# Kernel tuning notes

Hardware: AMD Instinct MI355X
Metric: run time of the kernel (lower is better)

The kernel has to match this reference:

```python
import jax, jax.numpy as jnp
import numpy as np

DOWNSAMPLE_RATIO = 4  # init kwarg


def farthest_point_sample(pos, m):
    """PointNet++-style FPS. pos: [B,N,3] float. Returns int32 indices [B,m].
    Starts from point 0, iteratively picks the point with max min-distance to
    the already-selected set (squared euclidean), matching the CUDA kernel."""
    B, N, _ = pos.shape

    def step(carry, _):
        dist, last = carry                                   # [B,N], [B]
        p = jnp.take_along_axis(pos, last[:, None, None], axis=1)  # [B,1,3]
        d = jnp.sum((pos - p) ** 2, axis=-1)                 # [B,N]
        dist = jnp.minimum(dist, d)
        nxt = jnp.argmax(dist, axis=-1).astype(jnp.int32)    # [B]
        return (dist, nxt), nxt

    idx0 = jnp.zeros((B,), jnp.int32)
    dist0 = jnp.full((B, N), 1e10, dtype=pos.dtype)
    _, rest = jax.lax.scan(step, (dist0, idx0), None, length=m - 1)  # rest: [m-1,B]
    return jnp.concatenate([idx0[None, :], rest], axis=0).T  # [B,m]


def setup_inputs() -> dict:
    key = jax.random.key(0)
    k1, k2 = jax.random.split(key)
    B, N, C = 8, 16384, 256
    pos = jax.random.normal(k1, (B, N, 3), dtype=jnp.float32)
    feat = jax.random.normal(k2, (B, N, C), dtype=jnp.float32)
    return {"pos": pos, "feat": feat}


def reference(pos, feat):
    # fps_preprocess is None -> run FPS then gather (gather_operation == index
    # select along the point dim; the einsum transposes in the original cancel).
    B, N, _ = pos.shape
    m = N // DOWNSAMPLE_RATIO
    idx = farthest_point_sample(pos, m)                      # [B,m] int32
    pos_ds = jnp.take_along_axis(pos, idx[:, :, None], axis=1)   # [B,m,3]
    feat_ds = jnp.take_along_axis(feat, idx[:, :, None], axis=1)  # [B,m,C]
    return (pos_ds, feat_ds)
```

## Files before the change

kernel.cpp:

```cpp
#include <hip/hip_runtime.h>
#include <hip/hip_bf16.h>


constexpr int NPTS   = 16384;
constexpr int PTS    = 16;
constexpr int FPS_T  = 1024;
constexpr int WAVES  = FPS_T / 64;

template <int CTRL>
__device__ __forceinline__ float dpp_f(float x) {
    return __builtin_bit_cast(float,
        __builtin_amdgcn_update_dpp(0, __builtin_bit_cast(int, x), CTRL, 0xF, 0xF, true));
}
template <int CTRL>
__device__ __forceinline__ int dpp_i(int x) {
    return __builtin_amdgcn_update_dpp(0, x, CTRL, 0xF, 0xF, true);
}

__device__ __forceinline__ void permswap16_f(float &a, float &b) {
    asm volatile("v_permlane16_swap_b32 %0, %1" : "+v"(a), "+v"(b));
}
__device__ __forceinline__ void permswap16_i(int &a, int &b) {
    asm volatile("v_permlane16_swap_b32 %0, %1" : "+v"(a), "+v"(b));
}
__device__ __forceinline__ void permswap32_f(float &a, float &b) {
    asm volatile("v_permlane32_swap_b32 %0, %1" : "+v"(a), "+v"(b));
}
__device__ __forceinline__ void permswap32_i(int &a, int &b) {
    asm volatile("v_permlane32_swap_b32 %0, %1" : "+v"(a), "+v"(b));
}

__device__ __forceinline__ void take(float &v, int &i, float ov, int oi) {
    bool t = (ov > v) || (ov == v && oi < i);
    v = t ? ov : v;
    i = t ? oi : i;
}

__global__ __launch_bounds__(FPS_T)
__attribute__((amdgpu_waves_per_eu(4, 4)))
void fps_kernel(
    const float* __restrict__ pos,
    float* __restrict__ pos_out,
    int* __restrict__ idx_out,
    int m)
{
    const int b    = blockIdx.x;
    const int t    = threadIdx.x;
    const int lane = t & 63;
    const int wid  = t >> 6;
    const bool l16 = (lane & 16) != 0;
    const bool l32 = (lane & 32) != 0;
    const float* posb = pos + (size_t)b * NPTS * 3;

    __shared__ float  s_v[2][WAVES];
    __shared__ int    s_i[2][WAVES];
    __shared__ float2 sxy[NPTS];

    float pz[PTS], dist[PTS];
#pragma unroll
    for (int j = 0; j < PTS; ++j) {
        const int i = j * FPS_T + t;
        sxy[i]  = make_float2(posb[i * 3 + 0], posb[i * 3 + 1]);
        pz[j]   = posb[i * 3 + 2];
        dist[j] = 1e10f;
    }

    float lx = posb[0], ly = posb[1], lz = posb[2];

    if (t == 0) {
        idx_out[(size_t)b * m] = 0;
        pos_out[((size_t)b * m) * 3 + 0] = lx;
        pos_out[((size_t)b * m) * 3 + 1] = ly;
        pos_out[((size_t)b * m) * 3 + 2] = lz;
    }
    __syncthreads();

    for (int s = 1; s < m; ++s) {
        float bv = -1.0f;
        int   bj = 0;
        {
#pragma clang fp contract(off)
#pragma unroll
            for (int j = 0; j < PTS; ++j) {
                float2 xy = sxy[j * FPS_T + t];
                float dx = xy.x - lx;
                float dy = xy.y - ly;
                float dz = pz[j] - lz;
                float d  = ((dx * dx) + (dy * dy)) + (dz * dz);
                float nd = fminf(dist[j], d);
                dist[j]  = nd;
                if (nd > bv) { bv = nd; bj = j; }
            }
        }
        int bi = bj * FPS_T + t;

        take(bv, bi, dpp_f<0xB1>(bv),  dpp_i<0xB1>(bi));
        take(bv, bi, dpp_f<0x4E>(bv),  dpp_i<0x4E>(bi));
        take(bv, bi, dpp_f<0x141>(bv), dpp_i<0x141>(bi));
        take(bv, bi, dpp_f<0x140>(bv), dpp_i<0x140>(bi));
        {
            float a = bv, c = bv; permswap16_f(a, c);
            int   e = bi, f = bi; permswap16_i(e, f);
            take(bv, bi, l16 ? a : c, l16 ? e : f);
        }
        {
            float a = bv, c = bv; permswap32_f(a, c);
            int   e = bi, f = bi; permswap32_i(e, f);
            take(bv, bi, l32 ? a : c, l32 ? e : f);
        }

        const int buf = s & 1;
        __syncthreads();
        if (lane == 0) { s_v[buf][wid] = bv; s_i[buf][wid] = bi; }
        __syncthreads();

        float gv = s_v[buf][lane & (WAVES - 1)];
        int   gi = s_i[buf][lane & (WAVES - 1)];
        take(gv, gi, dpp_f<0xB1>(gv),  dpp_i<0xB1>(gi));
        take(gv, gi, dpp_f<0x4E>(gv),  dpp_i<0x4E>(gi));
        take(gv, gi, dpp_f<0x141>(gv), dpp_i<0x141>(gi));
        take(gv, gi, dpp_f<0x140>(gv), dpp_i<0x140>(gi));

        int gis = __builtin_amdgcn_readfirstlane(gi);
        lx = posb[gis * 3 + 0];
        ly = posb[gis * 3 + 1];
        lz = posb[gis * 3 + 2];

        if (t == 0) {
            idx_out[(size_t)b * m + s] = gis;
            pos_out[((size_t)b * m + s) * 3 + 0] = lx;
            pos_out[((size_t)b * m + s) * 3 + 1] = ly;
            pos_out[((size_t)b * m + s) * 3 + 2] = lz;
        }
    }
}

__global__ __launch_bounds__(256) void gather_kernel(
    const float* __restrict__ feat,
    const int*   __restrict__ idx,
    float*       __restrict__ out,
    int m, int C)
{
    const int wid  = threadIdx.x >> 6;
    const int lane = threadIdx.x & 63;
    const int r    = blockIdx.x * 4 + wid;
    const int b    = r >> 12;
    const int src  = idx[r];
    const float4* sp = (const float4*)(feat + ((size_t)b * NPTS + src) * C);
    float4*       dp = (float4*)(out + (size_t)r * C);
    dp[lane] = sp[lane];
}

extern "C" void kernel_launch(void* const* d_in, const int* in_sizes, int n_in,
                              void* d_out, int out_size, void* d_ws, size_t ws_size,
                              hipStream_t stream) {
    const float* pos  = (const float*)d_in[0];
    const float* feat = (const float*)d_in[1];

    const int B = 8, C = 256;
    const int m = NPTS / 4;

    float* out_pos  = (float*)d_out;
    float* out_feat = out_pos + (size_t)B * m * 3;
    int*   idx      = (int*)d_ws;

    fps_kernel<<<dim3(B), dim3(FPS_T), 0, stream>>>(pos, out_pos, idx, m);
    gather_kernel<<<dim3(B * m / 4), dim3(256), 0, stream>>>(feat, idx, out_feat, m, C);
}
```

Baseline: 9.350 ms.

## Split FPS argmax into value-only max reduction then ballot-based index recovery

```diff
diff --git a/kernel.cpp b/kernel.cpp
--- a/kernel.cpp
+++ b/kernel.cpp
@@ -20,20 +20,8 @@
 __device__ __forceinline__ void permswap16_f(float &a, float &b) {
     asm volatile("v_permlane16_swap_b32 %0, %1" : "+v"(a), "+v"(b));
 }
-__device__ __forceinline__ void permswap16_i(int &a, int &b) {
-    asm volatile("v_permlane16_swap_b32 %0, %1" : "+v"(a), "+v"(b));
-}
 __device__ __forceinline__ void permswap32_f(float &a, float &b) {
     asm volatile("v_permlane32_swap_b32 %0, %1" : "+v"(a), "+v"(b));
-}
-__device__ __forceinline__ void permswap32_i(int &a, int &b) {
-    asm volatile("v_permlane32_swap_b32 %0, %1" : "+v"(a), "+v"(b));
-}
-
-__device__ __forceinline__ void take(float &v, int &i, float ov, int oi) {
-    bool t = (ov > v) || (ov == v && oi < i);
-    v = t ? ov : v;
-    i = t ? oi : i;
 }
 
 __global__ __launch_bounds__(FPS_T)
@@ -77,7 +65,6 @@
 
     for (int s = 1; s < m; ++s) {
         float bv = -1.0f;
-        int   bj = 0;
         {
 #pragma clang fp contract(off)
 #pragma unroll
@@ -89,37 +76,43 @@
                 float d  = ((dx * dx) + (dy * dy)) + (dz * dz);
                 float nd = fminf(dist[j], d);
                 dist[j]  = nd;
-                if (nd > bv) { bv = nd; bj = j; }
+                bv = fmaxf(bv, nd);
             }
         }
-        int bi = bj * FPS_T + t;
 
-        take(bv, bi, dpp_f<0xB1>(bv),  dpp_i<0xB1>(bi));
-        take(bv, bi, dpp_f<0x4E>(bv),  dpp_i<0x4E>(bi));
-        take(bv, bi, dpp_f<0x141>(bv), dpp_i<0x141>(bi));
-        take(bv, bi, dpp_f<0x140>(bv), dpp_i<0x140>(bi));
-        {
-            float a = bv, c = bv; permswap16_f(a, c);
-            int   e = bi, f = bi; permswap16_i(e, f);
-            take(bv, bi, l16 ? a : c, l16 ? e : f);
-        }
-        {
-            float a = bv, c = bv; permswap32_f(a, c);
-            int   e = bi, f = bi; permswap32_i(e, f);
-            take(bv, bi, l32 ? a : c, l32 ? e : f);
-        }
+        bv = fmaxf(bv, dpp_f<0xB1>(bv));
+        bv = fmaxf(bv, dpp_f<0x4E>(bv));
+        bv = fmaxf(bv, dpp_f<0x141>(bv));
+        bv = fmaxf(bv, dpp_f<0x140>(bv));
+        { float a = bv, c = bv; permswap16_f(a, c); bv = fmaxf(bv, l16 ? a : c); }
+        { float a = bv, c = bv; permswap32_f(a, c); bv = fmaxf(bv, l32 ? a : c); }
 
         const int buf = s & 1;
-        __syncthreads();
-        if (lane == 0) { s_v[buf][wid] = bv; s_i[buf][wid] = bi; }
+        if (lane == 0) s_v[buf][wid] = bv;
         __syncthreads();
 
         float gv = s_v[buf][lane & (WAVES - 1)];
-        int   gi = s_i[buf][lane & (WAVES - 1)];
-        take(gv, gi, dpp_f<0xB1>(gv),  dpp_i<0xB1>(gi));
-        take(gv, gi, dpp_f<0x4E>(gv),  dpp_i<0x4E>(gi));
-        take(gv, gi, dpp_f<0x141>(gv), dpp_i<0x141>(gi));
-        take(gv, gi, dpp_f<0x140>(gv), dpp_i<0x140>(gi));
+        gv = fmaxf(gv, dpp_f<0xB1>(gv));
+        gv = fmaxf(gv, dpp_f<0x4E>(gv));
+        gv = fmaxf(gv, dpp_f<0x141>(gv));
+        gv = fmaxf(gv, dpp_f<0x140>(gv));
+
+        int cand = 0x7FFFFFFF;
+#pragma unroll
+        for (int j = 0; j < PTS; ++j) {
+            unsigned long long mk = __ballot(dist[j] == gv);
+            if (cand == 0x7FFFFFFF && mk != 0ull)
+                cand = j * FPS_T + (wid << 6) + (int)__builtin_ctzll(mk);
+        }
+
+        if (lane == 0) s_i[buf][wid] = cand;
+        __syncthreads();
+
+        int gi = s_i[buf][lane & (WAVES - 1)];
+        { int o = dpp_i<0xB1>(gi);  gi = o < gi ? o : gi; }
+        { int o = dpp_i<0x4E>(gi);  gi = o < gi ? o : gi; }
+        { int o = dpp_i<0x141>(gi); gi = o < gi ? o : gi; }
+        { int o = dpp_i<0x140>(gi); gi = o < gi ? o : gi; }
 
         int gis = __builtin_amdgcn_readfirstlane(gi);
         lx = posb[gis * 3 + 0];
```

After: 10.02 ms. +7.2%, slower.
